# Kernel optimization log

Hardware: AMD Instinct MI355X
Metric: run time of the kernel (lower is better)

The kernel has to match this reference:

```python
import jax, jax.numpy as jnp
import numpy as np

N, IN_DIM, HID, HEADS, HOPS, NCLS, E = 20000, 1536, 256, 4, 3, 3, 320000
HD = HID // HEADS
EPS = 1e-5
NEG_SLOPE = 0.2


def layer_norm(x, g, b):
    mu = jnp.mean(x, axis=-1, keepdims=True)
    var = jnp.var(x, axis=-1, keepdims=True)
    return (x - mu) * jax.lax.rsqrt(var + EPS) * g + b


def gatv2(x, src, dst, Wl, bl, Wr, br, att, bias):
    # x: [N, HID]; src/dst: [E'] (self loops included)
    xl = (x @ Wl + bl).reshape(N, HEADS, HD)  # source transform
    xr = (x @ Wr + br).reshape(N, HEADS, HD)  # target transform
    e = jax.nn.leaky_relu(xl[src] + xr[dst], NEG_SLOPE)          # [E', H, D]
    logits = jnp.einsum('ehd,hd->eh', e, att)                     # [E', H]
    m = jax.ops.segment_max(logits, dst, num_segments=N)         # [N, H]
    ex = jnp.exp(logits - m[dst])
    denom = jax.ops.segment_sum(ex, dst, num_segments=N)
    alpha = ex / denom[dst]                                       # softmax per dst
    msg = xl[src] * alpha[:, :, None]                             # [E', H, D]
    out = jax.ops.segment_sum(msg, dst, num_segments=N)
    return out.reshape(N, HID) + bias


def setup_inputs() -> dict:
    key = jax.random.key(0)
    ks = jax.random.split(key, 20)
    s = lambda k, shp, sc: jax.random.normal(k, shp, jnp.float32) * sc
    return {
        'features': s(ks[0], (N, IN_DIM), 1.0),
        'edge_index': jax.random.randint(ks[1], (2, E), 0, N, jnp.int64),
        'proj_W': s(ks[2], (IN_DIM, HID), 0.02),
        'proj_b': jnp.zeros((HID,), jnp.float32),
        'n0_g': jnp.ones((HID,), jnp.float32),
        'n0_b': jnp.zeros((HID,), jnp.float32),
        'Wl': s(ks[3], (HOPS, HID, HID), 0.05),
        'bl': jnp.zeros((HOPS, HID), jnp.float32),
        'Wr': s(ks[4], (HOPS, HID, HID), 0.05),
        'br': jnp.zeros((HOPS, HID), jnp.float32),
        'att': s(ks[5], (HOPS, HEADS, HD), 0.1),
        'gbias': jnp.zeros((HOPS, HID), jnp.float32),
        'ln_g': jnp.ones((HOPS, HID), jnp.float32),
        'ln_b': jnp.zeros((HOPS, HID), jnp.float32),
        'h1_W': s(ks[6], (HID, HID), 0.05),
        'h1_b': jnp.zeros((HID,), jnp.float32),
        'h2_W': s(ks[7], (HID, NCLS), 0.05),
        'h2_b': jnp.zeros((NCLS,), jnp.float32),
    }


def reference(features, edge_index, proj_W, proj_b, n0_g, n0_b, Wl, bl, Wr, br,
              att, gbias, ln_g, ln_b, h1_W, h1_b, h2_W, h2_b):
    # add self loops (PyG GATv2Conv default)
    loop = jnp.arange(N, dtype=edge_index.dtype)
    src = jnp.concatenate([edge_index[0], loop])
    dst = jnp.concatenate([edge_index[1], loop])

    x = layer_norm(features @ proj_W + proj_b, n0_g, n0_b)
    for h in range(HOPS):
        g = gatv2(x, src, dst, Wl[h], bl[h], Wr[h], br[h], att[h], gbias[h])
        x = layer_norm(g + x, ln_g[h], ln_b[h])
    # head (dropout inactive at eval); torch GELU is exact erf form
    x = jax.nn.gelu(x @ h1_W + h1_b, approximate=False)
    return x @ h2_W + h2_b
```

## Files before the change

### kernel.cpp

```cpp
#include <hip/hip_runtime.h>
#include <hip/hip_bf16.h>
#include <math.h>

#define NN 20000
#define MPAD 20096
#define INDIM 1536
#define HID 256
#define NE 320000
#define NEDGE (NE + NN)
#define EPSV 1e-5f
#define NEG 0.2f

typedef unsigned short ushort_b;
typedef unsigned int uint32;
typedef __bf16 bf16x8 __attribute__((ext_vector_type(8)));
typedef float f32x4 __attribute__((ext_vector_type(4)));

#define AS1(p) ((const __attribute__((address_space(1))) void*)(p))
#define AS3(p) ((__attribute__((address_space(3))) void*)(p))

__device__ inline ushort_b f2bf(float x) {
  union { float f; uint32 u; } v; v.f = x;
  uint32 r = v.u + 0x7FFFu + ((v.u >> 16) & 1u);
  return (ushort_b)(r >> 16);
}
__device__ inline float bf2f(ushort_b h) {
  union { uint32 u; float f; } v; v.u = ((uint32)h) << 16;
  return v.f;
}
__device__ inline float4 ldbf4(const ushort_b* p) {
  ushort4 u = *(const ushort4*)p;
  float4 f;
  f.x = bf2f(u.x); f.y = bf2f(u.y); f.z = bf2f(u.z); f.w = bf2f(u.w);
  return f;
}

template<int AFP32, int OUTMODE>
__global__ __launch_bounds__(256) void gemm_mfma(
    const void* __restrict__ Av,
    const ushort_b* __restrict__ Bt0, const ushort_b* __restrict__ Bt1,
    const float* __restrict__ bias0, const float* __restrict__ bias1,
    void* __restrict__ C0, void* __restrict__ C1,
    int Mstore, int K)
{
  __shared__ ushort_b As[128 * 32];
  __shared__ ushort_b Bs[128 * 32];
  const ushort_b* Bt = blockIdx.z ? Bt1 : Bt0;
  const float* bias  = blockIdx.z ? bias1 : bias0;
  void* Cv           = blockIdx.z ? C1 : C0;

  int tid = threadIdx.x;
  int wave = tid >> 6, lane = tid & 63;
  int r0 = blockIdx.y * 128;
  int c0 = blockIdx.x * 128;
  int wm = (wave >> 1) << 6, wn = (wave & 1) << 6;
  int mrow = lane & 15, quad = lane >> 4;

  f32x4 acc[4][4] = {};

  for (int k0 = 0; k0 < K; k0 += 32) {
#pragma unroll
    for (int it = 0; it < 2; it++) {
      int off = (wave << 10) + (it << 12) + (lane << 4);
      int row = off >> 6;
      int colb = off & 63;
      const char* gB = (const char*)Bt + ((size_t)(c0 + row) * K + k0) * 2 + colb;
      __builtin_amdgcn_global_load_lds(AS1(gB), AS3((char*)Bs + off), 16, 0, 0);
    }
    if (AFP32) {
      const float* Af = (const float*)Av;
#pragma unroll
      for (int p = 0; p < 4; p++) {
        int off4 = (p << 8) + tid;
        int row = off4 >> 3, col4 = off4 & 7;
        float4 av = make_float4(0.f, 0.f, 0.f, 0.f);
        int grow = r0 + row;
        if (grow < Mstore) av = *(const float4*)(Af + (size_t)grow * K + k0 + (col4 << 2));
        uint2 u;
        u.x = (uint32)f2bf(av.x) | ((uint32)f2bf(av.y) << 16);
        u.y = (uint32)f2bf(av.z) | ((uint32)f2bf(av.w) << 16);
        *(uint2*)(As + (row << 5) + (col4 << 2)) = u;
      }
    } else {
      const ushort_b* Ab = (const ushort_b*)Av;
#pragma unroll
      for (int it = 0; it < 2; it++) {
        int off = (wave << 10) + (it << 12) + (lane << 4);
        int row = off >> 6;
        int colb = off & 63;
        const char* gA = (const char*)Ab + ((size_t)(r0 + row) * K + k0) * 2 + colb;
        __builtin_amdgcn_global_load_lds(AS1(gA), AS3((char*)As + off), 16, 0, 0);
      }
    }
    __syncthreads();

    bf16x8 af[4], bfr[4];
#pragma unroll
    for (int t = 0; t < 4; t++) {
      af[t]  = *(const bf16x8*)(As + ((wm + (t << 4) + mrow) << 5) + (quad << 3));
      bfr[t] = *(const bf16x8*)(Bs + ((wn + (t << 4) + mrow) << 5) + (quad << 3));
    }
#pragma unroll
    for (int mt = 0; mt < 4; mt++)
#pragma unroll
      for (int nt = 0; nt < 4; nt++)
        acc[mt][nt] = __builtin_amdgcn_mfma_f32_16x16x32_bf16(af[mt], bfr[nt], acc[mt][nt], 0, 0, 0);
    __syncthreads();
  }

#pragma unroll
  for (int nt = 0; nt < 4; nt++) {
    int col = c0 + wn + (nt << 4) + mrow;
    float bb = bias[col];
#pragma unroll
    for (int mt = 0; mt < 4; mt++) {
#pragma unroll
      for (int r = 0; r < 4; r++) {
        int row = r0 + wm + (mt << 4) + (quad << 2) + r;
        if (row < Mstore) {
          float v = acc[mt][nt][r] + bb;
          if (OUTMODE == 1) v = 0.5f * v * (1.f + erff(v * 0.70710678118654752f));
          if (OUTMODE == 2) ((ushort_b*)Cv)[(size_t)row * 256 + col] = f2bf(v);
          else              ((float*)Cv)[(size_t)row * 256 + col] = v;
        }
      }
    }
  }
}

__global__ __launch_bounds__(256) void transpose_cast(
    const float* __restrict__ in, ushort_b* __restrict__ out, int R, int C)
{
  __shared__ float t[32][33];
  int bx = blockIdx.x * 32;
  int by = blockIdx.y * 32;
  for (int i = threadIdx.y; i < 32; i += 8)
    t[i][threadIdx.x] = in[(size_t)(by + i) * C + bx + threadIdx.x];
  __syncthreads();
  for (int i = threadIdx.y; i < 32; i += 8)
    out[(size_t)(bx + i) * R + by + threadIdx.x] = f2bf(t[threadIdx.x][i]);
}

__global__ __launch_bounds__(256) void ln4_kernel(
    const float* __restrict__ in, const float* __restrict__ g,
    const float* __restrict__ b, float* __restrict__ out,
    ushort_b* __restrict__ bf_out, int n)
{
  int wave = threadIdx.x >> 6, lane = threadIdx.x & 63;
  int row = blockIdx.x * 4 + wave;
  if (row >= n) return;
  int c = lane << 2;
  float4 v = *(const float4*)(in + (size_t)row * HID + c);
  float s1 = v.x + v.y + v.z + v.w;
  float s2 = v.x * v.x + v.y * v.y + v.z * v.z + v.w * v.w;
#pragma unroll
  for (int m = 1; m < 64; m <<= 1) {
    s1 += __shfl_xor(s1, m, 64);
    s2 += __shfl_xor(s2, m, 64);
  }
  float mu = s1 * (1.f / 256.f);
  float var = s2 * (1.f / 256.f) - mu * mu;
  float rstd = rsqrtf(var + EPSV);
  float4 gv = *(const float4*)(g + c);
  float4 bv = *(const float4*)(b + c);
  float4 o;
  o.x = (v.x - mu) * rstd * gv.x + bv.x;
  o.y = (v.y - mu) * rstd * gv.y + bv.y;
  o.z = (v.z - mu) * rstd * gv.z + bv.z;
  o.w = (v.w - mu) * rstd * gv.w + bv.w;
  *(float4*)(out + (size_t)row * HID + c) = o;
  ushort4 ub;
  ub.x = f2bf(o.x); ub.y = f2bf(o.y); ub.z = f2bf(o.z); ub.w = f2bf(o.w);
  *(ushort4*)(bf_out + (size_t)row * HID + c) = ub;
}

__global__ void count_kernel(const int* __restrict__ ei, int* __restrict__ cnt)
{
  int e = blockIdx.x * blockDim.x + threadIdx.x;
  if (e < NEDGE) {
    int d = (e < NE) ? ei[NE + e] : (e - NE);
    atomicAdd(&cnt[d], 1);
  }
}

__global__ __launch_bounds__(1024) void scan_kernel(
    const int* __restrict__ cnt, int* __restrict__ offs, int* __restrict__ cursor)
{
  __shared__ int smem[1024];
  __shared__ int carry;
  int tid = threadIdx.x;
  if (tid == 0) carry = 0;
  __syncthreads();
  for (int base = 0; base < NN; base += 1024) {
    int v = (base + tid < NN) ? cnt[base + tid] : 0;
    smem[tid] = v;
    __syncthreads();
    for (int off = 1; off < 1024; off <<= 1) {
      int t = (tid >= off) ? smem[tid - off] : 0;
      __syncthreads();
      smem[tid] += t;
      __syncthreads();
    }
    int excl = smem[tid] - v + carry;
    if (base + tid < NN) { offs[base + tid] = excl; cursor[base + tid] = excl; }
    __syncthreads();
    if (tid == 0) carry += smem[1023];
    __syncthreads();
  }
  if (tid == 0) offs[NN] = NEDGE;
}

__global__ void scatter_kernel(const int* __restrict__ ei, int* __restrict__ cursor,
                               int* __restrict__ csr_src)
{
  int e = blockIdx.x * blockDim.x + threadIdx.x;
  if (e < NEDGE) {
    int s, d;
    if (e < NE) { s = ei[e]; d = ei[NE + e]; }
    else { s = e - NE; d = e - NE; }
    int p = atomicAdd(&cursor[d], 1);
    csr_src[p] = s;
  }
}

#define UPD(mS, lS, q0, q1, q2, q3, lg, xv) {      \
    float mn = fmaxf(mS, lg);                       \
    float sc = __expf(mS - mn);                     \
    float w  = __expf(lg - mn);                     \
    lS = lS * sc + w;                               \
    q0 = q0 * sc + w * xv.x;                        \
    q1 = q1 * sc + w * xv.y;                        \
    q2 = q2 * sc + w * xv.z;                        \
    q3 = q3 * sc + w * xv.w;                        \
    mS = mn; }

__device__ inline float edge_logit(float4 xv, float4 xrv, float4 attv) {
  float e0 = xv.x + xrv.x, e1 = xv.y + xrv.y, e2 = xv.z + xrv.z, e3 = xv.w + xrv.w;
  e0 = (e0 > 0.f) ? e0 : NEG * e0;
  e1 = (e1 > 0.f) ? e1 : NEG * e1;
  e2 = (e2 > 0.f) ? e2 : NEG * e2;
  e3 = (e3 > 0.f) ? e3 : NEG * e3;
  float lc = e0 * attv.x + e1 * attv.y + e2 * attv.z + e3 * attv.w;
  lc += __shfl_xor(lc, 1, 16);
  lc += __shfl_xor(lc, 2, 16);
  lc += __shfl_xor(lc, 4, 16);
  lc += __shfl_xor(lc, 8, 16);
  return lc;
}

__global__ __launch_bounds__(256) void gat_kernel(
    const ushort_b* __restrict__ xl, const ushort_b* __restrict__ xr,
    const float* __restrict__ x_in, const float* __restrict__ att,
    const float* __restrict__ gbias, const float* __restrict__ ln_g,
    const float* __restrict__ ln_b, const int* __restrict__ offs,
    const int* __restrict__ csr_src, float* __restrict__ x_out,
    ushort_b* __restrict__ xb_out)
{
  int wave = threadIdx.x >> 6, lane = threadIdx.x & 63;
  int node = blockIdx.x * 4 + wave;
  if (node >= NN) return;
  int c = lane << 2;
  float4 xrv = ldbf4(xr + (size_t)node * HID + c);
  float4 attv = *(const float4*)(att + c);

  float m1 = -INFINITY, l1 = 0.f, p10 = 0.f, p11 = 0.f, p12 = 0.f, p13 = 0.f;
  float m2 = -INFINITY, l2 = 0.f, p20 = 0.f, p21 = 0.f, p22 = 0.f, p23 = 0.f;

  int e = offs[node], end = offs[node + 1];
  for (; e + 1 < end; e += 2) {
    int s1 = csr_src[e], s2 = csr_src[e + 1];
    float4 xa = ldbf4(xl + (size_t)s1 * HID + c);
    float4 xb = ldbf4(xl + (size_t)s2 * HID + c);
    float la = edge_logit(xa, xrv, attv);
    float lb = edge_logit(xb, xrv, attv);
    UPD(m1, l1, p10, p11, p12, p13, la, xa);
    UPD(m2, l2, p20, p21, p22, p23, lb, xb);
  }
  if (e < end) {
    int s1 = csr_src[e];
    float4 xa = ldbf4(xl + (size_t)s1 * HID + c);
    float la = edge_logit(xa, xrv, attv);
    UPD(m1, l1, p10, p11, p12, p13, la, xa);
  }
  float mm = fmaxf(m1, m2);
  float sA = __expf(m1 - mm), sB = (m2 == -INFINITY) ? 0.f : __expf(m2 - mm);
  float l = l1 * sA + l2 * sB;
  float inv = 1.f / l;
  float a0 = (p10 * sA + p20 * sB) * inv;
  float a1 = (p11 * sA + p21 * sB) * inv;
  float a2 = (p12 * sA + p22 * sB) * inv;
  float a3 = (p13 * sA + p23 * sB) * inv;

  float4 xv = *(const float4*)(x_in + (size_t)node * HID + c);
  float4 gb = *(const float4*)(gbias + c);
  float o0 = a0 + gb.x + xv.x;
  float o1 = a1 + gb.y + xv.y;
  float o2 = a2 + gb.z + xv.z;
  float o3 = a3 + gb.w + xv.w;
  float s1s = o0 + o1 + o2 + o3;
  float s2s = o0 * o0 + o1 * o1 + o2 * o2 + o3 * o3;
#pragma unroll
  for (int mmk = 1; mmk < 64; mmk <<= 1) {
    s1s += __shfl_xor(s1s, mmk, 64);
    s2s += __shfl_xor(s2s, mmk, 64);
  }
  float mu = s1s * (1.f / 256.f);
  float var = s2s * (1.f / 256.f) - mu * mu;
  float rstd = rsqrtf(var + EPSV);
  float4 gv = *(const float4*)(ln_g + c);
  float4 bv = *(const float4*)(ln_b + c);
  float4 o;
  o.x = (o0 - mu) * rstd * gv.x + bv.x;
  o.y = (o1 - mu) * rstd * gv.y + bv.y;
  o.z = (o2 - mu) * rstd * gv.z + bv.z;
  o.w = (o3 - mu) * rstd * gv.w + bv.w;
  *(float4*)(x_out + (size_t)node * HID + c) = o;
  ushort4 ub;
  ub.x = f2bf(o.x); ub.y = f2bf(o.y); ub.z = f2bf(o.z); ub.w = f2bf(o.w);
  *(ushort4*)(xb_out + (size_t)node * HID + c) = ub;
}

__global__ __launch_bounds__(256) void head2_kernel(
    const float* __restrict__ t1, const float* __restrict__ W,
    const float* __restrict__ bias, float* __restrict__ out)
{
  int wave = threadIdx.x >> 6, lane = threadIdx.x & 63;
  int row = blockIdx.x * 4 + wave;
  if (row >= NN) return;
  int c = lane << 2;
  float4 v = *(const float4*)(t1 + (size_t)row * HID + c);
  float p0 = 0.f, p1 = 0.f, p2 = 0.f;
#pragma unroll
  for (int j = 0; j < 4; j++) {
    float vj = (&v.x)[j];
    p0 += vj * W[(c + j) * 3 + 0];
    p1 += vj * W[(c + j) * 3 + 1];
    p2 += vj * W[(c + j) * 3 + 2];
  }
#pragma unroll
  for (int mm = 1; mm < 64; mm <<= 1) {
    p0 += __shfl_xor(p0, mm, 64);
    p1 += __shfl_xor(p1, mm, 64);
    p2 += __shfl_xor(p2, mm, 64);
  }
  if (lane == 0) {
    out[(size_t)row * 3 + 0] = p0 + bias[0];
    out[(size_t)row * 3 + 1] = p1 + bias[1];
    out[(size_t)row * 3 + 2] = p2 + bias[2];
  }
}

extern "C" void kernel_launch(void* const* d_in, const int* in_sizes, int n_in,
                              void* d_out, int out_size, void* d_ws, size_t ws_size,
                              hipStream_t stream)
{
  const float* features = (const float*)d_in[0];
  const int*   ei       = (const int*)d_in[1];
  const float* proj_W   = (const float*)d_in[2];
  const float* proj_b   = (const float*)d_in[3];
  const float* n0_g     = (const float*)d_in[4];
  const float* n0_b     = (const float*)d_in[5];
  const float* Wl       = (const float*)d_in[6];
  const float* bl       = (const float*)d_in[7];
  const float* Wr       = (const float*)d_in[8];
  const float* br       = (const float*)d_in[9];
  const float* att      = (const float*)d_in[10];
  const float* gbias    = (const float*)d_in[11];
  const float* ln_g     = (const float*)d_in[12];
  const float* ln_b     = (const float*)d_in[13];
  const float* h1_W     = (const float*)d_in[14];
  const float* h1_b     = (const float*)d_in[15];
  const float* h2_W     = (const float*)d_in[16];
  const float* h2_b     = (const float*)d_in[17];
  float* out = (float*)d_out;

  char* w = (char*)d_ws;
  float*    x0   = (float*)w;    w += (size_t)NN * HID * 4;
  float*    x1   = (float*)w;    w += (size_t)NN * HID * 4;
  ushort_b* xlb  = (ushort_b*)w; w += (size_t)NN * HID * 2;
  ushort_b* xrb  = (ushort_b*)w; w += (size_t)NN * HID * 2;
  ushort_b* xb   = (ushort_b*)w; w += (size_t)MPAD * HID * 2;
  ushort_b* wtp  = (ushort_b*)w; w += (size_t)HID * INDIM * 2;
  ushort_b* wtl  = (ushort_b*)w; w += (size_t)3 * HID * HID * 2;
  ushort_b* wtr  = (ushort_b*)w; w += (size_t)3 * HID * HID * 2;
  ushort_b* wth1 = (ushort_b*)w; w += (size_t)HID * HID * 2;
  int* cnt    = (int*)w;  w += (size_t)NN * 4;
  int* offs   = (int*)w;  w += (size_t)(NN + 1) * 4;
  int* cursor = (int*)w;  w += (size_t)NN * 4;
  int* csr    = (int*)w;  w += (size_t)NEDGE * 4;

  hipMemsetAsync(cnt, 0, (size_t)NN * 4, stream);
  hipMemsetAsync(xb + (size_t)NN * HID, 0, (size_t)(MPAD - NN) * HID * 2, stream);
  count_kernel<<<(NEDGE + 255) / 256, 256, 0, stream>>>(ei, cnt);
  scan_kernel<<<1, 1024, 0, stream>>>(cnt, offs, cursor);
  scatter_kernel<<<(NEDGE + 255) / 256, 256, 0, stream>>>(ei, cursor, csr);

  transpose_cast<<<dim3(HID / 32, INDIM / 32), dim3(32, 8), 0, stream>>>(proj_W, wtp, INDIM, HID);
  for (int h = 0; h < 3; h++) {
    transpose_cast<<<dim3(HID / 32, HID / 32), dim3(32, 8), 0, stream>>>(
        Wl + (size_t)h * HID * HID, wtl + (size_t)h * HID * HID, HID, HID);
    transpose_cast<<<dim3(HID / 32, HID / 32), dim3(32, 8), 0, stream>>>(
        Wr + (size_t)h * HID * HID, wtr + (size_t)h * HID * HID, HID, HID);
  }
  transpose_cast<<<dim3(HID / 32, HID / 32), dim3(32, 8), 0, stream>>>(h1_W, wth1, HID, HID);

  dim3 gproj(2, MPAD / 128, 1);
  dim3 ghop(2, MPAD / 128, 2);

  gemm_mfma<1, 0><<<gproj, 256, 0, stream>>>(features, wtp, wtp, proj_b, proj_b,
                                             x1, x1, NN, INDIM);
  ln4_kernel<<<(NN + 3) / 4, 256, 0, stream>>>(x1, n0_g, n0_b, x0, xb, NN);

  float* xcur = x0;
  float* xnxt = x1;
  for (int h = 0; h < 3; h++) {
    gemm_mfma<0, 2><<<ghop, 256, 0, stream>>>(
        xb, wtl + (size_t)h * HID * HID, wtr + (size_t)h * HID * HID,
        bl + h * HID, br + h * HID, xlb, xrb, NN, HID);
    gat_kernel<<<(NN + 3) / 4, 256, 0, stream>>>(
        xlb, xrb, xcur, att + h * HID, gbias + h * HID,
        ln_g + h * HID, ln_b + h * HID, offs, csr, xnxt, xb);
    float* t = xcur; xcur = xnxt; xnxt = t;
  }

  gemm_mfma<0, 1><<<gproj, 256, 0, stream>>>(xb, wth1, wth1, h1_b, h1_b,
                                             xnxt, xnxt, NN, HID);
  head2_kernel<<<(NN + 3) / 4, 256, 0, stream>>>(xnxt, h2_W, h2_b, out);
}
```

Measured before the change: 660.7 us.

## Double-buffer GEMM LDS tiles and unroll GAT edge loop to four streams

The MFMA GEMM now uses two LDS buffers per operand. Loads for the next K-tile (direct global-to-LDS for bf16, register-staged for the fp32 A operand) are issued before computing the current tile, and one barrier per iteration is removed. Separately, the GAT aggregation loop keeps four independent online-softmax accumulators instead of two, so more gathers of xl rows are in flight at once. The cost is doubled LDS usage per GEMM block, extra registers for the staged fp32 A tiles and the wider accumulators, and a vmcnt(0) wait at the top of each iteration that may limit how much overlap is achieved.

```diff
diff --git a/kernel.cpp b/kernel.cpp
--- a/kernel.cpp
+++ b/kernel.cpp
@@ -43,8 +43,8 @@
     void* __restrict__ C0, void* __restrict__ C1,
     int Mstore, int K)
 {
-  __shared__ ushort_b As[128 * 32];
-  __shared__ ushort_b Bs[128 * 32];
+  __shared__ ushort_b As[2][128 * 32];
+  __shared__ ushort_b Bs[2][128 * 32];
   const ushort_b* Bt = blockIdx.z ? Bt1 : Bt0;
   const float* bias  = blockIdx.z ? bias1 : bias0;
   void* Cv           = blockIdx.z ? C1 : C0;
@@ -55,57 +55,89 @@
   int c0 = blockIdx.x * 128;
   int wm = (wave >> 1) << 6, wn = (wave & 1) << 6;
   int mrow = lane & 15, quad = lane >> 4;
+  int nk = K >> 5;
+
+  const float* Af = (const float*)Av;
+  const ushort_b* Ab = (const ushort_b*)Av;
 
   f32x4 acc[4][4] = {};
-
-  for (int k0 = 0; k0 < K; k0 += 32) {
+  float4 avA[2][4];
+
+  auto issueB = [&](int k0, int buf) {
 #pragma unroll
     for (int it = 0; it < 2; it++) {
       int off = (wave << 10) + (it << 12) + (lane << 4);
-      int row = off >> 6;
-      int colb = off & 63;
-      const char* gB = (const char*)Bt + ((size_t)(c0 + row) * K + k0) * 2 + colb;
-      __builtin_amdgcn_global_load_lds(AS1(gB), AS3((char*)Bs + off), 16, 0, 0);
-    }
-    if (AFP32) {
-      const float* Af = (const float*)Av;
-#pragma unroll
-      for (int p = 0; p < 4; p++) {
-        int off4 = (p << 8) + tid;
-        int row = off4 >> 3, col4 = off4 & 7;
-        float4 av = make_float4(0.f, 0.f, 0.f, 0.f);
-        int grow = r0 + row;
-        if (grow < Mstore) av = *(const float4*)(Af + (size_t)grow * K + k0 + (col4 << 2));
-        uint2 u;
-        u.x = (uint32)f2bf(av.x) | ((uint32)f2bf(av.y) << 16);
-        u.y = (uint32)f2bf(av.z) | ((uint32)f2bf(av.w) << 16);
-        *(uint2*)(As + (row << 5) + (col4 << 2)) = u;
+      int row = off >> 6, colb = off & 63;
+      const char* g = (const char*)Bt + ((size_t)(c0 + row) * K + k0) * 2 + colb;
+      __builtin_amdgcn_global_load_lds(AS1(g), AS3((char*)Bs[buf] + off), 16, 0, 0);
+    }
+  };
+  auto issueA = [&](int k0, int buf) {
+#pragma unroll
+    for (int it = 0; it < 2; it++) {
+      int off = (wave << 10) + (it << 12) + (lane << 4);
+      int row = off >> 6, colb = off & 63;
+      const char* g = (const char*)Ab + ((size_t)(r0 + row) * K + k0) * 2 + colb;
+      __builtin_amdgcn_global_load_lds(AS1(g), AS3((char*)As[buf] + off), 16, 0, 0);
+    }
+  };
+  auto loadA = [&](int k0, float4* dst) {
+#pragma unroll
+    for (int p = 0; p < 4; p++) {
+      int off4 = (p << 8) + tid;
+      int row = off4 >> 3, col4 = off4 & 7;
+      int grow = r0 + row;
+      dst[p] = (grow < Mstore) ? *(const float4*)(Af + (size_t)grow * K + k0 + (col4 << 2))
+                               : make_float4(0.f, 0.f, 0.f, 0.f);
+    }
+  };
+  auto writeA = [&](const float4* src, int buf) {
+#pragma unroll
+    for (int p = 0; p < 4; p++) {
+      int off4 = (p << 8) + tid;
+      int row = off4 >> 3, col4 = off4 & 7;
+      uint2 u;
+      u.x = (uint32)f2bf(src[p].x) | ((uint32)f2bf(src[p].y) << 16);
+      u.y = (uint32)f2bf(src[p].z) | ((uint32)f2bf(src[p].w) << 16);
+      *(uint2*)(As[buf] + (row << 5) + (col4 << 2)) = u;
+    }
+  };
+
+  if (AFP32) {
+    loadA(0, avA[0]);
+    issueB(0, 0);
+    if (nk > 1) loadA(32, avA[1]);
+    writeA(avA[0], 0);
+  } else {
+    issueA(0, 0);
+    issueB(0, 0);
+  }
+
+  for (int k = 0; k < nk; k++) {
+    asm volatile("s_waitcnt vmcnt(0)" ::: "memory");
+    __syncthreads();
+    int kn = k + 1;
+    if (kn < nk) {
+      issueB(kn << 5, kn & 1);
+      if (AFP32) {
+        writeA(avA[kn & 1], kn & 1);
+        if (kn + 1 < nk) loadA((kn + 1) << 5, avA[k & 1]);
+      } else {
+        issueA(kn << 5, kn & 1);
       }
-    } else {
-      const ushort_b* Ab = (const ushort_b*)Av;
-#pragma unroll
-      for (int it = 0; it < 2; it++) {
-        int off = (wave << 10) + (it << 12) + (lane << 4);
-        int row = off >> 6;
-        int colb = off & 63;
-        const char* gA = (const char*)Ab + ((size_t)(r0 + row) * K + k0) * 2 + colb;
-        __builtin_amdgcn_global_load_lds(AS1(gA), AS3((char*)As + off), 16, 0, 0);
-      }
-    }
-    __syncthreads();
-
+    }
+    int buf = k & 1;
     bf16x8 af[4], bfr[4];
 #pragma unroll
     for (int t = 0; t < 4; t++) {
-      af[t]  = *(const bf16x8*)(As + ((wm + (t << 4) + mrow) << 5) + (quad << 3));
-      bfr[t] = *(const bf16x8*)(Bs + ((wn + (t << 4) + mrow) << 5) + (quad << 3));
+      af[t]  = *(const bf16x8*)(As[buf] + ((wm + (t << 4) + mrow) << 5) + (quad << 3));
+      bfr[t] = *(const bf16x8*)(Bs[buf] + ((wn + (t << 4) + mrow) << 5) + (quad << 3));
     }
 #pragma unroll
     for (int mt = 0; mt < 4; mt++)
 #pragma unroll
       for (int nt = 0; nt < 4; nt++)
         acc[mt][nt] = __builtin_amdgcn_mfma_f32_16x16x32_bf16(af[mt], bfr[nt], acc[mt][nt], 0, 0, 0);
-    __syncthreads();
   }
 
 #pragma unroll
@@ -263,33 +295,49 @@
   float4 xrv = ldbf4(xr + (size_t)node * HID + c);
   float4 attv = *(const float4*)(att + c);
 
-  float m1 = -INFINITY, l1 = 0.f, p10 = 0.f, p11 = 0.f, p12 = 0.f, p13 = 0.f;
-  float m2 = -INFINITY, l2 = 0.f, p20 = 0.f, p21 = 0.f, p22 = 0.f, p23 = 0.f;
+  float mS[4], lS[4], pS[4][4];
+#pragma unroll
+  for (int i = 0; i < 4; i++) {
+    mS[i] = -INFINITY; lS[i] = 0.f;
+    pS[i][0] = pS[i][1] = pS[i][2] = pS[i][3] = 0.f;
+  }
 
   int e = offs[node], end = offs[node + 1];
-  for (; e + 1 < end; e += 2) {
-    int s1 = csr_src[e], s2 = csr_src[e + 1];
-    float4 xa = ldbf4(xl + (size_t)s1 * HID + c);
-    float4 xb = ldbf4(xl + (size_t)s2 * HID + c);
-    float la = edge_logit(xa, xrv, attv);
-    float lb = edge_logit(xb, xrv, attv);
-    UPD(m1, l1, p10, p11, p12, p13, la, xa);
-    UPD(m2, l2, p20, p21, p22, p23, lb, xb);
-  }
-  if (e < end) {
-    int s1 = csr_src[e];
-    float4 xa = ldbf4(xl + (size_t)s1 * HID + c);
-    float la = edge_logit(xa, xrv, attv);
-    UPD(m1, l1, p10, p11, p12, p13, la, xa);
-  }
-  float mm = fmaxf(m1, m2);
-  float sA = __expf(m1 - mm), sB = (m2 == -INFINITY) ? 0.f : __expf(m2 - mm);
-  float l = l1 * sA + l2 * sB;
+  for (; e + 3 < end; e += 4) {
+    int s0 = csr_src[e], s1 = csr_src[e + 1], s2 = csr_src[e + 2], s3 = csr_src[e + 3];
+    float4 x0v = ldbf4(xl + (size_t)s0 * HID + c);
+    float4 x1v = ldbf4(xl + (size_t)s1 * HID + c);
+    float4 x2v = ldbf4(xl + (size_t)s2 * HID + c);
+    float4 x3v = ldbf4(xl + (size_t)s3 * HID + c);
+    float g0 = edge_logit(x0v, xrv, attv);
+    float g1 = edge_logit(x1v, xrv, attv);
+    float g2 = edge_logit(x2v, xrv, attv);
+    float g3 = edge_logit(x3v, xrv, attv);
+    UPD(mS[0], lS[0], pS[0][0], pS[0][1], pS[0][2], pS[0][3], g0, x0v);
+    UPD(mS[1], lS[1], pS[1][0], pS[1][1], pS[1][2], pS[1][3], g1, x1v);
+    UPD(mS[2], lS[2], pS[2][0], pS[2][1], pS[2][2], pS[2][3], g2, x2v);
+    UPD(mS[3], lS[3], pS[3][0], pS[3][1], pS[3][2], pS[3][3], g3, x3v);
+  }
+  for (; e < end; e++) {
+    int s0 = csr_src[e];
+    float4 x0v = ldbf4(xl + (size_t)s0 * HID + c);
+    float g0 = edge_logit(x0v, xrv, attv);
+    UPD(mS[0], lS[0], pS[0][0], pS[0][1], pS[0][2], pS[0][3], g0, x0v);
+  }
+
+  float mm = fmaxf(fmaxf(mS[0], mS[1]), fmaxf(mS[2], mS[3]));
+  float l = 0.f, a0 = 0.f, a1 = 0.f, a2 = 0.f, a3 = 0.f;
+#pragma unroll
+  for (int i = 0; i < 4; i++) {
+    float sc = (mS[i] == -INFINITY) ? 0.f : __expf(mS[i] - mm);
+    l  += lS[i] * sc;
+    a0 += pS[i][0] * sc;
+    a1 += pS[i][1] * sc;
+    a2 += pS[i][2] * sc;
+    a3 += pS[i][3] * sc;
+  }
   float inv = 1.f / l;
-  float a0 = (p10 * sA + p20 * sB) * inv;
-  float a1 = (p11 * sA + p21 * sB) * inv;
-  float a2 = (p12 * sA + p22 * sB) * inv;
-  float a3 = (p13 * sA + p23 * sB) * inv;
+  a0 *= inv; a1 *= inv; a2 *= inv; a3 *= inv;
 
   float4 xv = *(const float4*)(x_in + (size_t)node * HID + c);
   float4 gb = *(const float4*)(gbias + c);
```

Result: slower. 750.1 us (+13.5%).
